# Kernel tuning notes

Measured on AMD Instinct MI355X. Metric: run time of the kernel, lower is better.

Reference implementation:

```python
import jax, jax.numpy as jnp
import numpy as np

N, IN_CH, HIDDEN, HEADS, NUM_CLASSES, E = 50000, 128, 16, 8, 10, 800000
NEG_SLOPE = 0.2


def setup_inputs() -> dict:
    key = jax.random.key(0)
    ks = jax.random.split(key, 12)
    HC = HIDDEN * HEADS
    s = 0.1
    return {
        "x": jax.random.normal(ks[0], (N, IN_CH), dtype=jnp.float32),
        "edge_index": jax.random.randint(ks[1], (2, E), 0, N, dtype=jnp.int64),
        "W1": jax.random.normal(ks[2], (IN_CH, HC), dtype=jnp.float32) * s,
        "a_src1": jax.random.normal(ks[3], (HEADS, HIDDEN), dtype=jnp.float32) * s,
        "a_dst1": jax.random.normal(ks[4], (HEADS, HIDDEN), dtype=jnp.float32) * s,
        "b1": jnp.zeros((HC,), dtype=jnp.float32),
        "W2": jax.random.normal(ks[5], (HC, HC), dtype=jnp.float32) * s,
        "a_src2": jax.random.normal(ks[6], (HEADS, HIDDEN), dtype=jnp.float32) * s,
        "a_dst2": jax.random.normal(ks[7], (HEADS, HIDDEN), dtype=jnp.float32) * s,
        "b2": jnp.zeros((HC,), dtype=jnp.float32),
        "Wout": jax.random.normal(ks[8], (HC, NUM_CLASSES), dtype=jnp.float32) * s,
        "bout": jnp.zeros((NUM_CLASSES,), dtype=jnp.float32),
    }


def gat_layer(x, W, a_src, a_dst, b, src, dst):
    # h: [N, H, C] projected per-head features
    h = (x @ W).reshape(N, HEADS, HIDDEN)
    alpha_s = jnp.einsum("nhc,hc->nh", h, a_src)  # [N, H]
    alpha_d = jnp.einsum("nhc,hc->nh", h, a_dst)
    e = jax.nn.leaky_relu(alpha_s[src] + alpha_d[dst], NEG_SLOPE)  # [E2, H]
    # segment softmax over edges grouped by destination node
    m = jax.ops.segment_max(e, dst, num_segments=N)[dst]
    ex = jnp.exp(e - m)
    denom = jax.ops.segment_sum(ex, dst, num_segments=N)[dst]
    alpha = ex / denom  # [E2, H]
    out = jax.ops.segment_sum(alpha[:, :, None] * h[src], dst, num_segments=N)
    return out.reshape(N, HEADS * HIDDEN) + b


def reference(x, edge_index, W1, a_src1, a_dst1, b1, W2, a_src2, a_dst2, b2, Wout, bout):
    # PyG GATConv default: add self loops
    loops = jnp.arange(N, dtype=edge_index.dtype)
    src = jnp.concatenate([edge_index[0], loops])
    dst = jnp.concatenate([edge_index[1], loops])
    h = gat_layer(x, W1, a_src1, a_dst1, b1, src, dst)
    h = jax.nn.relu(h)  # norm=Identity, dropout inactive (eval)
    h = gat_layer(h, W2, a_src2, a_dst2, b2, src, dst)
    h = jax.nn.relu(h)
    return h @ Wout + bout
```

## Files before the change

kernel.cpp:

```cpp
#include <hip/hip_runtime.h>
#include <hip/hip_bf16.h>

#define NN 50000
#define EE 800000
#define E2 850000
#define HC 128
#define HEADS 8
#define HID 16
#define NC 10
#define NEG_SLOPE 0.2f

#define SCAN_B 256
#define NBLK ((NN + SCAN_B - 1) / SCAN_B)

__device__ inline unsigned pack_bf16x2(float x, float y) {
    unsigned ux = __float_as_uint(x); ux = (ux + 0x7FFFu + ((ux >> 16) & 1u)) >> 16;
    unsigned uy = __float_as_uint(y); uy = (uy + 0x7FFFu + ((uy >> 16) & 1u)) >> 16;
    return ux | (uy << 16);
}
__device__ inline float bf_lo(unsigned u) { return __uint_as_float(u << 16); }
__device__ inline float bf_hi(unsigned u) { return __uint_as_float(u & 0xFFFF0000u); }

__global__ __launch_bounds__(256) void count_deg_kernel(
    const int* __restrict__ ei, int* __restrict__ deg)
{
    int e = blockIdx.x * 256 + threadIdx.x;
    if (e >= E2) return;
    int dst = (e < EE) ? ei[EE + e] : (e - EE);
    atomicAdd(&deg[dst], 1);
}

__global__ __launch_bounds__(SCAN_B) void scan1_kernel(
    const int* __restrict__ deg, int* __restrict__ rowptr, int* __restrict__ bsum)
{
    __shared__ int sm[SCAN_B];
    const int b = blockIdx.x, t = threadIdx.x, i = b * SCAN_B + t;
    int v = (i < NN) ? deg[i] : 0;
    sm[t] = v;
    __syncthreads();
    for (int off = 1; off < SCAN_B; off <<= 1) {
        int x = (t >= off) ? sm[t - off] : 0;
        __syncthreads();
        sm[t] += x;
        __syncthreads();
    }
    if (i < NN) rowptr[i] = sm[t] - v;
    if (t == SCAN_B - 1) bsum[b] = sm[t];
}

__global__ __launch_bounds__(SCAN_B) void scan2_kernel(
    int* __restrict__ bsum, int* __restrict__ rowptr)
{
    __shared__ int sm[SCAN_B];
    const int t = threadIdx.x;
    int v = (t < NBLK) ? bsum[t] : 0;
    sm[t] = v;
    __syncthreads();
    for (int off = 1; off < SCAN_B; off <<= 1) {
        int x = (t >= off) ? sm[t - off] : 0;
        __syncthreads();
        sm[t] += x;
        __syncthreads();
    }
    if (t < NBLK) bsum[t] = sm[t] - v;
    if (t == NBLK - 1) rowptr[NN] = sm[t];
}

__global__ __launch_bounds__(SCAN_B) void scan3_kernel(
    int* __restrict__ rowptr, int* __restrict__ wo, const int* __restrict__ bsum)
{
    const int b = blockIdx.x, i = b * SCAN_B + threadIdx.x;
    if (i < NN) {
        int r = rowptr[i] + bsum[b];
        rowptr[i] = r;
        wo[i] = r;
    }
}

__global__ __launch_bounds__(256) void scatter_kernel(
    const int* __restrict__ ei, int* __restrict__ wo,
    int* __restrict__ srcs)
{
    int e = blockIdx.x * 256 + threadIdx.x;
    if (e >= E2) return;
    int src, dst;
    if (e < EE) { src = ei[e]; dst = ei[EE + e]; }
    else        { src = e - EE; dst = e - EE; }
    int pos = atomicAdd(&wo[dst], 1);
    srcs[pos] = src;
}

__global__ __launch_bounds__(512) void gemm_fused_kernel(
    const float* __restrict__ X, const float* __restrict__ W,
    const float* __restrict__ asrc, const float* __restrict__ adst,
    unsigned* __restrict__ Hb, float* __restrict__ AS, float* __restrict__ AD)
{
    __shared__ float Ws[8 * 2052];
    __shared__ float Xst[128 * 128];
    const int tid = threadIdx.x;
    const int row0 = blockIdx.x * 128;

    for (int i = tid; i < 4096; i += 512) {
        int k = i >> 5, q = i & 31;
        float4 v = ((const float4*)W)[i];
        *(float4*)&Ws[(q >> 2) * 2052 + k * 16 + (q & 3) * 4] = v;
    }
    {
        int r = tid & 127, quarter = tid >> 7;
        int row = row0 + r;
        if (row < NN) {
            const float4* xr = (const float4*)(X + (size_t)row * HC + quarter * 32);
            #pragma unroll
            for (int c4 = 0; c4 < 8; ++c4) {
                float4 v = xr[c4];
                int c = quarter * 32 + c4 * 4;
                Xst[(c + 0) * 128 + r] = v.x;
                Xst[(c + 1) * 128 + r] = v.y;
                Xst[(c + 2) * 128 + r] = v.z;
                Xst[(c + 3) * 128 + r] = v.w;
            }
        } else {
            #pragma unroll
            for (int c4 = 0; c4 < 8; ++c4) {
                int c = quarter * 32 + c4 * 4;
                Xst[(c + 0) * 128 + r] = 0.f;
                Xst[(c + 1) * 128 + r] = 0.f;
                Xst[(c + 2) * 128 + r] = 0.f;
                Xst[(c + 3) * 128 + r] = 0.f;
            }
        }
    }
    __syncthreads();

    const int rg = tid >> 3;
    const int head = tid & 7;
    float acc[2][16];
    #pragma unroll
    for (int i = 0; i < 2; ++i)
        #pragma unroll
        for (int j = 0; j < 16; ++j) acc[i][j] = 0.f;

    const float* wbase = &Ws[head * 2052];
    #pragma unroll 4
    for (int k = 0; k < 128; ++k) {
        float2 xv = *(const float2*)&Xst[k * 128 + rg * 2];
        const float* wp = wbase + k * 16;
        float4 w0 = *(const float4*)(wp + 0);
        float4 w1 = *(const float4*)(wp + 4);
        float4 w2 = *(const float4*)(wp + 8);
        float4 w3 = *(const float4*)(wp + 12);
        float xs[2] = {xv.x, xv.y};
        float ww[16] = {w0.x, w0.y, w0.z, w0.w, w1.x, w1.y, w1.z, w1.w,
                        w2.x, w2.y, w2.z, w2.w, w3.x, w3.y, w3.z, w3.w};
        #pragma unroll
        for (int i = 0; i < 2; ++i)
            #pragma unroll
            for (int j = 0; j < 16; ++j)
                acc[i][j] = fmaf(xs[i], ww[j], acc[i][j]);
    }

    #pragma unroll
    for (int i = 0; i < 2; ++i) {
        int row = row0 + rg * 2 + i;
        if (row >= NN) continue;
        unsigned* hp = Hb + (size_t)row * 64 + head * 8;
        uint4 p0 = make_uint4(pack_bf16x2(acc[i][0],  acc[i][1]),
                              pack_bf16x2(acc[i][2],  acc[i][3]),
                              pack_bf16x2(acc[i][4],  acc[i][5]),
                              pack_bf16x2(acc[i][6],  acc[i][7]));
        uint4 p1 = make_uint4(pack_bf16x2(acc[i][8],  acc[i][9]),
                              pack_bf16x2(acc[i][10], acc[i][11]),
                              pack_bf16x2(acc[i][12], acc[i][13]),
                              pack_bf16x2(acc[i][14], acc[i][15]));
        ((uint4*)hp)[0] = p0;
        ((uint4*)hp)[1] = p1;
        float s = 0.f, d = 0.f;
        #pragma unroll
        for (int j = 0; j < 16; ++j) {
            s = fmaf(acc[i][j], asrc[head * HID + j], s);
            d = fmaf(acc[i][j], adst[head * HID + j], d);
        }
        AS[row * HEADS + head] = s;
        AD[row * HEADS + head] = d;
    }
}

__global__ __launch_bounds__(256) void aggregate_kernel(
    const unsigned* __restrict__ Hb, const float* __restrict__ AS,
    const float* __restrict__ AD, const int* __restrict__ srcs,
    const int* __restrict__ rowptr, const float* __restrict__ bias,
    float* __restrict__ Out)
{
    const int wave = threadIdx.x >> 6;
    const int lane = threadIdx.x & 63;
    const int n = blockIdx.x * 4 + wave;
    if (n >= NN) return;
    const int head = lane >> 3;
    const int beg = rowptr[n], end = rowptr[n + 1];
    const float adv = AD[n * HEADS + head];

    float a0x = 0.f, a0y = 0.f, a1x = 0.f, a1y = 0.f;
    float a2x = 0.f, a2y = 0.f, a3x = 0.f, a3y = 0.f;
    float d0 = 0.f, d1 = 0.f, d2 = 0.f, d3 = 0.f;

    int s = beg;
    for (; s + 3 < end; s += 4) {
        int s0 = srcs[s], s1 = srcs[s + 1], s2 = srcs[s + 2], s3 = srcs[s + 3];
        float e0 = AS[s0 * HEADS + head] + adv;
        float e1 = AS[s1 * HEADS + head] + adv;
        float e2 = AS[s2 * HEADS + head] + adv;
        float e3 = AS[s3 * HEADS + head] + adv;
        unsigned h0 = Hb[(size_t)s0 * 64 + lane];
        unsigned h1 = Hb[(size_t)s1 * 64 + lane];
        unsigned h2 = Hb[(size_t)s2 * 64 + lane];
        unsigned h3 = Hb[(size_t)s3 * 64 + lane];
        e0 = (e0 >= 0.f) ? e0 : NEG_SLOPE * e0;
        e1 = (e1 >= 0.f) ? e1 : NEG_SLOPE * e1;
        e2 = (e2 >= 0.f) ? e2 : NEG_SLOPE * e2;
        e3 = (e3 >= 0.f) ? e3 : NEG_SLOPE * e3;
        float w0 = __expf(e0), w1 = __expf(e1), w2 = __expf(e2), w3 = __expf(e3);
        d0 += w0; d1 += w1; d2 += w2; d3 += w3;
        a0x = fmaf(w0, bf_lo(h0), a0x); a0y = fmaf(w0, bf_hi(h0), a0y);
        a1x = fmaf(w1, bf_lo(h1), a1x); a1y = fmaf(w1, bf_hi(h1), a1y);
        a2x = fmaf(w2, bf_lo(h2), a2x); a2y = fmaf(w2, bf_hi(h2), a2y);
        a3x = fmaf(w3, bf_lo(h3), a3x); a3y = fmaf(w3, bf_hi(h3), a3y);
    }
    for (; s < end; ++s) {
        int s0 = srcs[s];
        float e0 = AS[s0 * HEADS + head] + adv;
        unsigned h0 = Hb[(size_t)s0 * 64 + lane];
        e0 = (e0 >= 0.f) ? e0 : NEG_SLOPE * e0;
        float w0 = __expf(e0);
        d0 += w0;
        a0x = fmaf(w0, bf_lo(h0), a0x); a0y = fmaf(w0, bf_hi(h0), a0y);
    }
    float den = (d0 + d1) + (d2 + d3);
    float ax = (a0x + a1x) + (a2x + a3x);
    float ay = (a0y + a1y) + (a2y + a3y);
    float2 bv = *(const float2*)&bias[2 * lane];
    float ox = fmaxf(ax / den + bv.x, 0.f);
    float oy = fmaxf(ay / den + bv.y, 0.f);
    *(float2*)&Out[(size_t)n * HC + 2 * lane] = make_float2(ox, oy);
}

__global__ __launch_bounds__(256) void out_gemm_kernel(
    const float* __restrict__ X, const float* __restrict__ W,
    const float* __restrict__ b, float* __restrict__ Out)
{
    __shared__ float Ws[HC * NC];
    __shared__ float bs[NC];
    for (int i = threadIdx.x; i < HC * NC; i += 256) Ws[i] = W[i];
    if (threadIdx.x < NC) bs[threadIdx.x] = b[threadIdx.x];
    __syncthreads();
    int row = blockIdx.x * 256 + threadIdx.x;
    if (row >= NN) return;
    float acc[NC];
    #pragma unroll
    for (int j = 0; j < NC; ++j) acc[j] = bs[j];
    const float4* xr = (const float4*)(X + (size_t)row * HC);
    #pragma unroll 8
    for (int k4 = 0; k4 < 32; ++k4) {
        float4 v = xr[k4];
        const float* w0 = &Ws[(k4 * 4 + 0) * NC];
        const float* w1 = &Ws[(k4 * 4 + 1) * NC];
        const float* w2 = &Ws[(k4 * 4 + 2) * NC];
        const float* w3 = &Ws[(k4 * 4 + 3) * NC];
        #pragma unroll
        for (int j = 0; j < NC; ++j)
            acc[j] += v.x * w0[j] + v.y * w1[j] + v.z * w2[j] + v.w * w3[j];
    }
    float* op = Out + (size_t)row * NC;
    #pragma unroll
    for (int j = 0; j < NC; ++j) op[j] = acc[j];
}

extern "C" void kernel_launch(void* const* d_in, const int* in_sizes, int n_in,
                              void* d_out, int out_size, void* d_ws, size_t ws_size,
                              hipStream_t stream)
{
    const float* x      = (const float*)d_in[0];
    const int*   ei     = (const int*)d_in[1];
    const float* W1     = (const float*)d_in[2];
    const float* asrc1  = (const float*)d_in[3];
    const float* adst1  = (const float*)d_in[4];
    const float* b1     = (const float*)d_in[5];
    const float* W2     = (const float*)d_in[6];
    const float* asrc2  = (const float*)d_in[7];
    const float* adst2  = (const float*)d_in[8];
    const float* b2     = (const float*)d_in[9];
    const float* Wout   = (const float*)d_in[10];
    const float* bout   = (const float*)d_in[11];
    float* out = (float*)d_out;

    const size_t need_bytes =
        (size_t)NN * 64 * sizeof(unsigned) +
        ((size_t)NN * HC + (size_t)NN * HEADS * 2) * sizeof(float) +
        ((size_t)(NN + 1) + NN + NN + E2 + NBLK) * sizeof(int);
    if (ws_size < need_bytes) return;

    unsigned* hb = (unsigned*)d_ws;
    float* x2  = (float*)(hb + (size_t)NN * 64);
    float* as_ = x2 + (size_t)NN * HC;
    float* ad_ = as_ + (size_t)NN * HEADS;
    int* rowptr = (int*)(ad_ + (size_t)NN * HEADS);
    int* wo     = rowptr + (NN + 1);
    int* deg    = wo + NN;
    int* srcs   = deg + NN;
    int* bsum   = srcs + E2;

    const int egrid = (E2 + 255) / 256;

    hipMemsetAsync(deg, 0, NN * sizeof(int), stream);
    count_deg_kernel<<<egrid, 256, 0, stream>>>(ei, deg);
    scan1_kernel<<<NBLK, SCAN_B, 0, stream>>>(deg, rowptr, bsum);
    scan2_kernel<<<1, SCAN_B, 0, stream>>>(bsum, rowptr);
    scan3_kernel<<<NBLK, SCAN_B, 0, stream>>>(rowptr, wo, bsum);
    scatter_kernel<<<egrid, 256, 0, stream>>>(ei, wo, srcs);

    const int ggrid = (NN + 127) / 128;
    const int agrid = (NN + 3) / 4;

    gemm_fused_kernel<<<ggrid, 512, 0, stream>>>(x, W1, asrc1, adst1, hb, as_, ad_);
    aggregate_kernel<<<agrid, 256, 0, stream>>>(hb, as_, ad_, srcs, rowptr, b1, x2);

    gemm_fused_kernel<<<ggrid, 512, 0, stream>>>(x2, W2, asrc2, adst2, hb, as_, ad_);
    aggregate_kernel<<<agrid, 256, 0, stream>>>(hb, as_, ad_, srcs, rowptr, b2, x2);

    out_gemm_kernel<<<(NN + 255) / 256, 256, 0, stream>>>(x2, Wout, bout, out);
}
```

Baseline: 382.9 us.

## Build CSR with per-block shared-memory histograms instead of global atomics

Replaces the global-atomic degree count and scatter with a two-pass partitioned counting sort. 64 blocks each build shared-memory histograms over two halves of the node range, and column sums plus per-block offsets give each block its own write positions. The aim is to remove contended global atomics and make the CSR order deterministic within each block. The cost is only 64 blocks doing the edge work (low parallelism on a large GPU), a 64xN offsets table, and two extra kernels.

```diff
diff --git a/kernel.cpp b/kernel.cpp
--- a/kernel.cpp
+++ b/kernel.cpp
@@ -13,6 +13,10 @@
 #define SCAN_B 256
 #define NBLK ((NN + SCAN_B - 1) / SCAN_B)
 
+#define P 64
+#define CHUNK ((E2 + P - 1) / P)
+#define HALF 25000
+
 __device__ inline unsigned pack_bf16x2(float x, float y) {
     unsigned ux = __float_as_uint(x); ux = (ux + 0x7FFFu + ((ux >> 16) & 1u)) >> 16;
     unsigned uy = __float_as_uint(y); uy = (uy + 0x7FFFu + ((uy >> 16) & 1u)) >> 16;
@@ -21,13 +25,38 @@
 __device__ inline float bf_lo(unsigned u) { return __uint_as_float(u << 16); }
 __device__ inline float bf_hi(unsigned u) { return __uint_as_float(u & 0xFFFF0000u); }
 
-__global__ __launch_bounds__(256) void count_deg_kernel(
-    const int* __restrict__ ei, int* __restrict__ deg)
-{
-    int e = blockIdx.x * 256 + threadIdx.x;
-    if (e >= E2) return;
-    int dst = (e < EE) ? ei[EE + e] : (e - EE);
-    atomicAdd(&deg[dst], 1);
+__global__ __launch_bounds__(256) void hist_kernel(
+    const int* __restrict__ ei, int* __restrict__ Hh)
+{
+    __shared__ int hist[HALF];
+    const int b = blockIdx.x, t = threadIdx.x;
+    const int e0 = b * CHUNK;
+    const int e1 = min(e0 + CHUNK, E2);
+    for (int pass = 0; pass < 2; ++pass) {
+        const int base = pass * HALF;
+        for (int i = t; i < HALF; i += 256) hist[i] = 0;
+        __syncthreads();
+        for (int e = e0 + t; e < e1; e += 256) {
+            int dst = (e < EE) ? ei[EE + e] : (e - EE);
+            int d = dst - base;
+            if (d >= 0 && d < HALF) atomicAdd(&hist[d], 1);
+        }
+        __syncthreads();
+        int* outp = Hh + (size_t)b * NN + base;
+        for (int i = t; i < HALF; i += 256) outp[i] = hist[i];
+        __syncthreads();
+    }
+}
+
+__global__ __launch_bounds__(256) void colsum_kernel(
+    const int* __restrict__ Hh, int* __restrict__ deg)
+{
+    int n = blockIdx.x * 256 + threadIdx.x;
+    if (n >= NN) return;
+    int s = 0;
+    #pragma unroll 8
+    for (int b = 0; b < P; ++b) s += Hh[(size_t)b * NN + n];
+    deg[n] = s;
 }
 
 __global__ __launch_bounds__(SCAN_B) void scan1_kernel(
@@ -67,27 +96,52 @@
 }
 
 __global__ __launch_bounds__(SCAN_B) void scan3_kernel(
-    int* __restrict__ rowptr, int* __restrict__ wo, const int* __restrict__ bsum)
+    int* __restrict__ rowptr, const int* __restrict__ bsum)
 {
     const int b = blockIdx.x, i = b * SCAN_B + threadIdx.x;
-    if (i < NN) {
-        int r = rowptr[i] + bsum[b];
-        rowptr[i] = r;
-        wo[i] = r;
-    }
-}
-
-__global__ __launch_bounds__(256) void scatter_kernel(
-    const int* __restrict__ ei, int* __restrict__ wo,
+    if (i < NN) rowptr[i] += bsum[b];
+}
+
+__global__ __launch_bounds__(256) void offset_kernel(
+    int* __restrict__ Hh, const int* __restrict__ rowptr)
+{
+    int n = blockIdx.x * 256 + threadIdx.x;
+    if (n >= NN) return;
+    int run = rowptr[n];
+    #pragma unroll 8
+    for (int b = 0; b < P; ++b) {
+        size_t idx = (size_t)b * NN + n;
+        int c = Hh[idx];
+        Hh[idx] = run;
+        run += c;
+    }
+}
+
+__global__ __launch_bounds__(256) void scatter2_kernel(
+    const int* __restrict__ ei, const int* __restrict__ Hh,
     int* __restrict__ srcs)
 {
-    int e = blockIdx.x * 256 + threadIdx.x;
-    if (e >= E2) return;
-    int src, dst;
-    if (e < EE) { src = ei[e]; dst = ei[EE + e]; }
-    else        { src = e - EE; dst = e - EE; }
-    int pos = atomicAdd(&wo[dst], 1);
-    srcs[pos] = src;
+    __shared__ int hist[HALF];
+    const int b = blockIdx.x, t = threadIdx.x;
+    const int e0 = b * CHUNK;
+    const int e1 = min(e0 + CHUNK, E2);
+    const int* offp = Hh + (size_t)b * NN;
+    for (int pass = 0; pass < 2; ++pass) {
+        const int base = pass * HALF;
+        for (int i = t; i < HALF; i += 256) hist[i] = 0;
+        __syncthreads();
+        for (int e = e0 + t; e < e1; e += 256) {
+            int src, dst;
+            if (e < EE) { src = ei[e]; dst = ei[EE + e]; }
+            else        { src = e - EE; dst = e - EE; }
+            int d = dst - base;
+            if (d >= 0 && d < HALF) {
+                int rank = atomicAdd(&hist[d], 1);
+                srcs[offp[dst] + rank] = src;
+            }
+        }
+        __syncthreads();
+    }
 }
 
 __global__ __launch_bounds__(512) void gemm_fused_kernel(
@@ -295,7 +349,7 @@
     const size_t need_bytes =
         (size_t)NN * 64 * sizeof(unsigned) +
         ((size_t)NN * HC + (size_t)NN * HEADS * 2) * sizeof(float) +
-        ((size_t)(NN + 1) + NN + NN + E2 + NBLK) * sizeof(int);
+        ((size_t)(NN + 1) + NN + E2 + NBLK + (size_t)P * NN) * sizeof(int);
     if (ws_size < need_bytes) return;
 
     unsigned* hb = (unsigned*)d_ws;
@@ -303,19 +357,18 @@
     float* as_ = x2 + (size_t)NN * HC;
     float* ad_ = as_ + (size_t)NN * HEADS;
     int* rowptr = (int*)(ad_ + (size_t)NN * HEADS);
-    int* wo     = rowptr + (NN + 1);
-    int* deg    = wo + NN;
+    int* deg    = rowptr + (NN + 1);
     int* srcs   = deg + NN;
     int* bsum   = srcs + E2;
-
-    const int egrid = (E2 + 255) / 256;
-
-    hipMemsetAsync(deg, 0, NN * sizeof(int), stream);
-    count_deg_kernel<<<egrid, 256, 0, stream>>>(ei, deg);
+    int* Hh     = bsum + NBLK;
+
+    hist_kernel<<<P, 256, 0, stream>>>(ei, Hh);
+    colsum_kernel<<<(NN + 255) / 256, 256, 0, stream>>>(Hh, deg);
     scan1_kernel<<<NBLK, SCAN_B, 0, stream>>>(deg, rowptr, bsum);
     scan2_kernel<<<1, SCAN_B, 0, stream>>>(bsum, rowptr);
-    scan3_kernel<<<NBLK, SCAN_B, 0, stream>>>(rowptr, wo, bsum);
-    scatter_kernel<<<egrid, 256, 0, stream>>>(ei, wo, srcs);
+    scan3_kernel<<<NBLK, SCAN_B, 0, stream>>>(rowptr, bsum);
+    offset_kernel<<<(NN + 255) / 256, 256, 0, stream>>>(Hh, rowptr);
+    scatter2_kernel<<<P, 256, 0, stream>>>(ei, Hh, srcs);
 
     const int ggrid = (NN + 127) / 128;
     const int agrid = (NN + 3) / 4;
```

Result: slower. 397.0 us (+3.7%).
